# Optimization experiments

Hardware: AMD Instinct MI355X
Metric: run time of the kernel (lower is better)

## Reference

```python
import jax, jax.numpy as jnp
import numpy as np

B, L = 4, 2048
D_MODEL, D_STATE, D_CONV, EXPAND = 1024, 16, 4, 2
D_INNER = D_MODEL * EXPAND


def setup_inputs() -> dict:
    key = jax.random.key(0)
    ks = jax.random.split(key, 6)
    x = jax.random.normal(ks[0], (B, L, D_MODEL), dtype=jnp.float32)
    W_in = jax.random.normal(ks[1], (D_MODEL, 2 * D_INNER), dtype=jnp.float32) / np.sqrt(D_MODEL)
    conv_w = jax.random.normal(ks[2], (D_INNER, D_CONV), dtype=jnp.float32) / np.sqrt(D_CONV)
    conv_b = jax.random.normal(ks[3], (D_INNER,), dtype=jnp.float32) * 0.02
    W_x = jax.random.normal(ks[4], (D_INNER, 2 * D_STATE + 1), dtype=jnp.float32) / np.sqrt(D_INNER)
    A_log = jnp.log(jnp.arange(1, D_STATE + 1, dtype=jnp.float32))
    D_param = jnp.ones((D_INNER,), dtype=jnp.float32)
    W_out = jax.random.normal(ks[5], (D_INNER, D_MODEL), dtype=jnp.float32) / np.sqrt(D_INNER)
    return {"x": x, "W_in": W_in, "conv_w": conv_w, "conv_b": conv_b,
            "W_x": W_x, "A_log": A_log, "D_param": D_param, "W_out": W_out}


def _silu(v):
    return v * jax.nn.sigmoid(v)


def reference(x, W_in, conv_w, conv_b, W_x, A_log, D_param, W_out):
    b, l, _ = x.shape
    # input projection and split into ssm branch and gate
    xz = x @ W_in                                   # (b, l, 2*d_inner)
    x_ssm, z = jnp.split(xz, 2, axis=-1)            # each (b, l, d_inner)
    # depthwise causal conv1d (kernel D_CONV, left pad D_CONV-1, truncate to l)
    xp = jnp.pad(x_ssm, ((0, 0), (D_CONV - 1, 0), (0, 0)))
    xc = conv_b
    for k in range(D_CONV):                         # small fixed kernel loop
        xc = xc + xp[:, k:k + l, :] * conv_w[:, k]
    xc = _silu(xc)                                  # (b, l, d_inner)
    # input-dependent delta, B, C
    x_dbl = xc @ W_x                                # (b, l, 2*d_state+1)
    delta = jax.nn.softplus(x_dbl[..., :1])         # (b, l, 1)
    B_mat = x_dbl[..., 1:1 + D_STATE]               # (b, l, n)
    C_mat = x_dbl[..., 1 + D_STATE:]                # (b, l, n)
    A = -jnp.exp(A_log)                             # (n,)
    A_bar = jnp.exp(delta * A)                      # (b, l, n)
    B_bar = delta * B_mat                           # (b, l, n)

    def step(h, inp):
        a, bb, xt, ct = inp                         # (b,n),(b,n),(b,d),(b,n)
        h = a[:, None, :] * h + bb[:, None, :] * xt[:, :, None]  # (b,d,n)
        y = jnp.einsum('bdn,bn->bd', h, ct)
        return h, y

    h0 = jnp.zeros((b, D_INNER, D_STATE), dtype=x.dtype)
    seq = (jnp.swapaxes(A_bar, 0, 1), jnp.swapaxes(B_bar, 0, 1),
           jnp.swapaxes(xc, 0, 1), jnp.swapaxes(C_mat, 0, 1))
    _, ys = jax.lax.scan(step, h0, seq)             # (l, b, d_inner)
    y = jnp.swapaxes(ys, 0, 1)
    y = y + xc * D_param                            # skip connection
    y = y * _silu(z)                                # gating
    return y @ W_out                                # (b, l, d_model)
```

## Files before the change

### kernel.cpp

```cpp
#include <hip/hip_runtime.h>
#include <hip/hip_bf16.h>
#include <math.h>

typedef __hip_bfloat16 bf16;
typedef __attribute__((ext_vector_type(8))) short short8;
typedef __attribute__((ext_vector_type(4))) float f32x4;

#define BATCH   4
#define L_SEQ   2048
#define DMODEL  1024
#define DSTATE  16
#define DCONV   4
#define DINNER  2048
#define M_ROWS  (BATCH * L_SEQ)

#define CHUNK   64
#define NCH     (L_SEQ / CHUNK)
#define PSTR    52
#define NX      33
#define KSPL    4

__device__ __forceinline__ float b2f(bf16 v) { return __bfloat162float(v); }
__device__ __forceinline__ bf16  f2b(float v) { return __float2bfloat16(v); }
__device__ __forceinline__ float us2f(unsigned short u) {
    return __uint_as_float(((unsigned)u) << 16);
}
__device__ __forceinline__ float ldany(const void* p, int i, int f32) {
    return f32 ? ((const float*)p)[i] : b2f(((const bf16*)p)[i]);
}
__device__ __forceinline__ void load_lds16(const void* g, void* l) {
    __builtin_amdgcn_global_load_lds(
        (const __attribute__((address_space(1))) unsigned int*)g,
        (__attribute__((address_space(3))) unsigned int*)l, 16, 0, 0);
}

union V8 { float4 f4; unsigned short us[8]; };

__global__ void detect_dtype(const unsigned int* __restrict__ alog_bits,
                             int* __restrict__ flag)
{
    *flag = (alog_bits[0] == 0u) ? 1 : 0;
}

__global__ __launch_bounds__(256) void convert_bf16(
    const void* __restrict__ src, bf16* __restrict__ dst, int n,
    const int* __restrict__ flag)
{
    const int f = *flag;
    int i = blockIdx.x * 256 + threadIdx.x;
    if (i < n) dst[i] = f2b(ldany(src, i, f));
}

__global__ __launch_bounds__(256) void transpose_any(
    const void* __restrict__ src, bf16* __restrict__ dst,
    int R, int C, const int* __restrict__ flag)
{
    const int f = *flag;
    __shared__ float tile[32][33];
    int tx = threadIdx.x & 31;
    int ty = threadIdx.x >> 5;
    int c0 = blockIdx.x * 32;
    int r0 = blockIdx.y * 32;
    #pragma unroll
    for (int i = 0; i < 4; i++) {
        int r = r0 + ty + i * 8;
        tile[ty + i * 8][tx] = ldany(src, r * C + c0 + tx, f);
    }
    __syncthreads();
    #pragma unroll
    for (int i = 0; i < 4; i++) {
        int cr = c0 + ty + i * 8;
        dst[(size_t)cr * R + r0 + tx] = f2b(tile[tx][ty + i * 8]);
    }
}

__global__ __launch_bounds__(256) void gemm_mfma(
    const bf16* __restrict__ A, const bf16* __restrict__ Bt,
    void* __restrict__ C1v, void* __restrict__ C2v,
    int M, int N, int Kfull, int split,
    const int* __restrict__ flag, int oMode, int K)
{
    const int fo = (oMode == 2) ? 1 : (oMode & *flag);
    __shared__ __align__(16) bf16 As[128 * 32];
    __shared__ __align__(16) bf16 Bs[128 * 32];
    const int tid  = threadIdx.x;
    const int lane = tid & 63;
    const int w    = tid >> 6;
    const int wr   = w & 1, wc = w >> 1;
    const int m0   = blockIdx.y * 128;
    const int n0   = blockIdx.x * 128;
    const int kz   = blockIdx.z;
    const int kst  = kz * K;

    void* C1 = C1v;
    void* C2 = C2v;
    if (kz) { C1 = (char*)C1v + (size_t)kz * M * N * 4; C2 = C1; }

    f32x4 acc[4][4] = {};

    const int ldr = lane >> 2;
    const int ldc = (lane & 3) * 8;
    const int mrow = lane & 15;
    const int qk   = (lane >> 4) * 8;

    for (int k0 = kst; k0 < kst + K; k0 += 32) {
        __syncthreads();
        #pragma unroll
        for (int j = 0; j < 2; j++) {
            int rg = w * 2 + j;
            int r  = rg * 16 + ldr;
            load_lds16(A  + (size_t)(m0 + r) * Kfull + k0 + ldc, (char*)As + rg * 1024);
            load_lds16(Bt + (size_t)(n0 + r) * Kfull + k0 + ldc, (char*)Bs + rg * 1024);
        }
        __syncthreads();

        short8 af[4], bfr[4];
        #pragma unroll
        for (int i = 0; i < 4; i++) {
            af[i]  = *(const short8*)&As[(wr * 64 + i * 16 + mrow) * 32 + qk];
            bfr[i] = *(const short8*)&Bs[(wc * 64 + i * 16 + mrow) * 32 + qk];
        }
        #pragma unroll
        for (int mi = 0; mi < 4; mi++)
            #pragma unroll
            for (int ni = 0; ni < 4; ni++)
                acc[mi][ni] = __builtin_amdgcn_mfma_f32_16x16x32_bf16(
                    af[mi], bfr[ni], acc[mi][ni], 0, 0, 0);
    }

    const int orow = m0 + wr * 64 + (lane >> 4) * 4;
    const int ocol = wc * 64 + (lane & 15);

    if (n0 + 128 <= split) {
        if (fo) {
            float* Cp = (float*)C1 + (size_t)orow * split + n0 + ocol;
            #pragma unroll
            for (int mi = 0; mi < 4; mi++)
                #pragma unroll
                for (int ni = 0; ni < 4; ni++)
                    #pragma unroll
                    for (int r = 0; r < 4; r++)
                        Cp[(size_t)(mi * 16 + r) * split + ni * 16] = acc[mi][ni][r];
        } else {
            bf16* Cp = (bf16*)C1 + (size_t)orow * split + n0 + ocol;
            #pragma unroll
            for (int mi = 0; mi < 4; mi++)
                #pragma unroll
                for (int ni = 0; ni < 4; ni++)
                    #pragma unroll
                    for (int r = 0; r < 4; r++)
                        Cp[(size_t)(mi * 16 + r) * split + ni * 16] = f2b(acc[mi][ni][r]);
        }
    } else if (n0 >= split) {
        const int Nc = N - split;
        if (fo) {
            float* Cp = (float*)C2 + (size_t)orow * Nc + (n0 - split) + ocol;
            #pragma unroll
            for (int mi = 0; mi < 4; mi++)
                #pragma unroll
                for (int ni = 0; ni < 4; ni++)
                    #pragma unroll
                    for (int r = 0; r < 4; r++)
                        Cp[(size_t)(mi * 16 + r) * Nc + ni * 16] = acc[mi][ni][r];
        } else {
            bf16* Cp = (bf16*)C2 + (size_t)orow * Nc + (n0 - split) + ocol;
            #pragma unroll
            for (int mi = 0; mi < 4; mi++)
                #pragma unroll
                for (int ni = 0; ni < 4; ni++)
                    #pragma unroll
                    for (int r = 0; r < 4; r++)
                        Cp[(size_t)(mi * 16 + r) * Nc + ni * 16] = f2b(acc[mi][ni][r]);
        }
    } else {
        #pragma unroll
        for (int mi = 0; mi < 4; mi++)
            #pragma unroll
            for (int ni = 0; ni < 4; ni++)
                #pragma unroll
                for (int r = 0; r < 4; r++) {
                    int row = orow + mi * 16 + r;
                    int col = n0 + ocol + ni * 16;
                    if (col >= N) continue;
                    float v = acc[mi][ni][r];
                    if (col < split) {
                        if (fo) ((float*)C1)[(size_t)row * split + col] = v;
                        else    ((bf16*)C1)[(size_t)row * split + col]  = f2b(v);
                    } else {
                        int c2 = col - split;
                        if (fo) ((float*)C2)[(size_t)row * (N - split) + c2] = v;
                        else    ((bf16*)C2)[(size_t)row * (N - split) + c2]  = f2b(v);
                    }
                }
    }
}

#define CLC 16

__global__ __launch_bounds__(256) void conv_silu_kernel(
    const bf16* __restrict__ x_ssm, const void* __restrict__ conv_w,
    const void* __restrict__ conv_b, bf16* __restrict__ xc,
    const int* __restrict__ flag)
{
    const int f   = *flag;
    const int tid = threadIdx.x;
    const int d0  = tid * 8;
    const int b   = blockIdx.x / (L_SEQ / CLC);
    const int l0  = (blockIdx.x % (L_SEQ / CLC)) * CLC;

    float wk[DCONV][8], bias[8];
    #pragma unroll
    for (int j = 0; j < 8; j++) {
        bias[j] = ldany(conv_b, d0 + j, f);
        #pragma unroll
        for (int k = 0; k < DCONV; k++)
            wk[k][j] = ldany(conv_w, (d0 + j) * DCONV + k, f);
    }

    const size_t rowstr = DINNER;
    const unsigned short* xin = (const unsigned short*)x_ssm;

    float win[3][8];
    #pragma unroll
    for (int r = 0; r < 3; r++) {
        int l = l0 - 3 + r;
        if (l >= 0) {
            V8 v; v.f4 = *(const float4*)(xin + ((size_t)(b * L_SEQ + l)) * rowstr + d0);
            #pragma unroll
            for (int j = 0; j < 8; j++) win[r][j] = us2f(v.us[j]);
        } else {
            #pragma unroll
            for (int j = 0; j < 8; j++) win[r][j] = 0.f;
        }
    }

    #pragma unroll
    for (int t = 0; t < CLC; t++) {
        int l = l0 + t;
        V8 v; v.f4 = *(const float4*)(xin + ((size_t)(b * L_SEQ + l)) * rowstr + d0);
        float cur[8];
        #pragma unroll
        for (int j = 0; j < 8; j++) cur[j] = us2f(v.us[j]);

        V8 o;
        #pragma unroll
        for (int j = 0; j < 8; j++) {
            float s = bias[j];
            s = fmaf(wk[0][j], win[0][j], s);
            s = fmaf(wk[1][j], win[1][j], s);
            s = fmaf(wk[2][j], win[2][j], s);
            s = fmaf(wk[3][j], cur[j],    s);
            float sv = s / (1.f + __expf(-s));
            o.us[j] = (unsigned short)(__bfloat16_as_ushort(f2b(sv)));
        }
        *(float4*)((unsigned short*)xc + ((size_t)(b * L_SEQ + l)) * rowstr + d0) = o.f4;

        #pragma unroll
        for (int j = 0; j < 8; j++) {
            win[0][j] = win[1][j];
            win[1][j] = win[2][j];
            win[2][j] = cur[j];
        }
    }
}

__global__ void transpose_wx(const void* __restrict__ W_x, bf16* __restrict__ W_xT,
                             const int* __restrict__ flag)
{
    const int f = *flag;
    int idx = blockIdx.x * 256 + threadIdx.x;
    if (idx >= NX * DINNER) return;
    int n = idx / DINNER;
    int k = idx - n * DINNER;
    W_xT[idx] = f2b(ldany(W_x, k * NX + n, f));
}

__global__ __launch_bounds__(256) void pack_P(
    const float* __restrict__ xdbl, const void* __restrict__ A_log,
    float* __restrict__ P, const int* __restrict__ flag)
{
    const int f = *flag;
    int i  = blockIdx.x * 256 + threadIdx.x;
    int bl = i >> 4, n = i & 15;
    float x0 = 0.f, bn = 0.f, cn = 0.f;
    #pragma unroll
    for (int s = 0; s < KSPL; s++) {
        const float* row = xdbl + (size_t)s * M_ROWS * NX + (size_t)bl * NX;
        x0 += row[0];
        bn += row[1 + n];
        cn += row[17 + n];
    }
    float delta = (x0 > 20.f) ? x0 : log1pf(expf(x0));
    float Aneg = -expf(ldany(A_log, n, f));
    float* p = P + (size_t)bl * PSTR;
    p[n]      = expf(delta * Aneg);
    p[16 + n] = delta * bn;
    p[32 + n] = cn;
    if (n == 0) p[48] = delta;
}

__global__ __launch_bounds__(256) void scan_phase1(
    const float* __restrict__ P, const bf16* __restrict__ xc,
    float* __restrict__ hstate)
{
    const int blk = blockIdx.x;
    const int b = blk >> 8;
    const int c = (blk >> 3) & 31;
    const int g = blk & 7;
    const int tid = threadIdx.x;
    const int d = g * 256 + tid;

    __shared__ __align__(16) unsigned short sX[CHUNK][256];

    #pragma unroll
    for (int r = 0; r < 16; r++) {
        int i = r * 256 + tid;
        int t = i >> 6;
        int dd = (i & 63) * 4;
        *(ushort4*)&sX[t][dd] = *(const ushort4*)((const unsigned short*)xc +
            ((size_t)(b * L_SEQ) + c * CHUNK + t) * DINNER + g * 256 + dd);
    }
    __syncthreads();

    const float* __restrict__ p = P + ((size_t)(b * L_SEQ) + c * CHUNK) * PSTR;

    float h[16];
    #pragma unroll
    for (int n = 0; n < 16; n++) h[n] = 0.f;

    #pragma unroll 4
    for (int t = 0; t < CHUNK; t++) {
        const float* pt = p + (size_t)t * PSTR;
        float4 a0 = *(const float4*)(pt + 0);
        float4 a1 = *(const float4*)(pt + 4);
        float4 a2 = *(const float4*)(pt + 8);
        float4 a3 = *(const float4*)(pt + 12);
        float4 b0 = *(const float4*)(pt + 16);
        float4 b1 = *(const float4*)(pt + 20);
        float4 b2 = *(const float4*)(pt + 24);
        float4 b3 = *(const float4*)(pt + 28);
        float xv = us2f(sX[t][tid]);
        float av[16] = {a0.x,a0.y,a0.z,a0.w, a1.x,a1.y,a1.z,a1.w,
                        a2.x,a2.y,a2.z,a2.w, a3.x,a3.y,a3.z,a3.w};
        float bv[16] = {b0.x,b0.y,b0.z,b0.w, b1.x,b1.y,b1.z,b1.w,
                        b2.x,b2.y,b2.z,b2.w, b3.x,b3.y,b3.z,b3.w};
        #pragma unroll
        for (int n = 0; n < 16; n++)
            h[n] = fmaf(av[n], h[n], bv[n] * xv);
    }
    float* out = hstate + (((size_t)b * NCH + c) * DINNER + d) * 16;
    #pragma unroll
    for (int q = 0; q < 4; q++)
        *(float4*)&out[q * 4] = *(const float4*)&h[q * 4];
}

__global__ __launch_bounds__(64) void sum_delta(const float* __restrict__ P,
                                                float* __restrict__ S)
{
    int i = blockIdx.x;
    int t = threadIdx.x;
    float v = P[((size_t)((i >> 5) * L_SEQ) + (i & 31) * CHUNK + t) * PSTR + 48];
    #pragma unroll
    for (int off = 32; off > 0; off >>= 1)
        v += __shfl_xor(v, off);
    if (t == 0) S[i] = v;
}

__global__ __launch_bounds__(256) void scan_phase2(
    float* __restrict__ hstate, const float* __restrict__ S,
    const void* __restrict__ A_log, const int* __restrict__ flag)
{
    const int f = *flag;
    const int b = blockIdx.x >> 7;
    const int dg = blockIdx.x & 127;
    const int tid = threadIdx.x;
    const int d = dg * 16 + (tid >> 4);
    const int n = tid & 15;
    const float Aneg = -expf(ldany(A_log, n, f));

    __shared__ float sS[NCH];
    if (tid < NCH) sS[tid] = S[b * NCH + tid];
    __syncthreads();

    float H = 0.f;
    size_t base = ((size_t)b * NCH * DINNER + d) * 16 + n;
    for (int c = 0; c < NCH; c++) {
        size_t idx = base + (size_t)c * (DINNER * 16);
        float hend = hstate[idx];
        hstate[idx] = H;
        H = fmaf(__expf(Aneg * sS[c]), H, hend);
    }
}

__global__ __launch_bounds__(256) void scan_phase3(
    const float* __restrict__ P, const bf16* __restrict__ xc,
    const bf16* __restrict__ z, const void* __restrict__ Dp,
    const float* __restrict__ hstate, bf16* __restrict__ y,
    const int* __restrict__ flag)
{
    const int f = *flag;
    const int blk = blockIdx.x;
    const int b = blk >> 8;
    const int c = (blk >> 3) & 31;
    const int g = blk & 7;
    const int tid = threadIdx.x;
    const int d = g * 256 + tid;

    __shared__ __align__(16) unsigned short sX[CHUNK][256];

    #pragma unroll
    for (int r = 0; r < 16; r++) {
        int i = r * 256 + tid;
        int t = i >> 6;
        int dd = (i & 63) * 4;
        *(ushort4*)&sX[t][dd] = *(const ushort4*)((const unsigned short*)xc +
            ((size_t)(b * L_SEQ) + c * CHUNK + t) * DINNER + g * 256 + dd);
    }
    __syncthreads();

    const float Dd = ldany(Dp, d, f);
    float h[16];
    const float* hin = hstate + (((size_t)b * NCH + c) * DINNER + d) * 16;
    #pragma unroll
    for (int q = 0; q < 4; q++)
        *(float4*)&h[q * 4] = *(const float4*)&hin[q * 4];

    const float* __restrict__ p = P + ((size_t)(b * L_SEQ) + c * CHUNK) * PSTR;
    const size_t ybase = ((size_t)(b * L_SEQ) + c * CHUNK) * DINNER + d;
    const unsigned short* zp = (const unsigned short*)z;

    #pragma unroll 4
    for (int t = 0; t < CHUNK; t++) {
        const float* pt = p + (size_t)t * PSTR;
        float4 a0 = *(const float4*)(pt + 0);
        float4 a1 = *(const float4*)(pt + 4);
        float4 a2 = *(const float4*)(pt + 8);
        float4 a3 = *(const float4*)(pt + 12);
        float4 b0 = *(const float4*)(pt + 16);
        float4 b1 = *(const float4*)(pt + 20);
        float4 b2 = *(const float4*)(pt + 24);
        float4 b3 = *(const float4*)(pt + 28);
        float4 c0 = *(const float4*)(pt + 32);
        float4 c1 = *(const float4*)(pt + 36);
        float4 c2 = *(const float4*)(pt + 40);
        float4 c3 = *(const float4*)(pt + 44);
        float xv = us2f(sX[t][tid]);
        float av[16] = {a0.x,a0.y,a0.z,a0.w, a1.x,a1.y,a1.z,a1.w,
                        a2.x,a2.y,a2.z,a2.w, a3.x,a3.y,a3.z,a3.w};
        float bv[16] = {b0.x,b0.y,b0.z,b0.w, b1.x,b1.y,b1.z,b1.w,
                        b2.x,b2.y,b2.z,b2.w, b3.x,b3.y,b3.z,b3.w};
        float cv[16] = {c0.x,c0.y,c0.z,c0.w, c1.x,c1.y,c1.z,c1.w,
                        c2.x,c2.y,c2.z,c2.w, c3.x,c3.y,c3.z,c3.w};
        float p0 = 0.f, p1 = 0.f;
        #pragma unroll
        for (int n = 0; n < 16; n += 2) {
            h[n]     = fmaf(av[n],     h[n],     bv[n]     * xv);
            h[n + 1] = fmaf(av[n + 1], h[n + 1], bv[n + 1] * xv);
            p0 = fmaf(h[n],     cv[n],     p0);
            p1 = fmaf(h[n + 1], cv[n + 1], p1);
        }
        float zv = us2f(zp[ybase + (size_t)t * DINNER]);
        float yv = (p0 + p1) + xv * Dd;
        float sz = zv / (1.f + __expf(-zv));
        y[ybase + (size_t)t * DINNER] = f2b(yv * sz);
    }
}

extern "C" void kernel_launch(void* const* d_in, const int* in_sizes, int n_in,
                              void* d_out, int out_size, void* d_ws, size_t ws_size,
                              hipStream_t stream)
{
    const void* x      = d_in[0];
    const void* W_in   = d_in[1];
    const void* conv_w = d_in[2];
    const void* conv_b = d_in[3];
    const void* W_x    = d_in[4];
    const void* A_log  = d_in[5];
    const void* Dp     = d_in[6];
    const void* W_out  = d_in[7];

    char* w = (char*)d_ws;
    bf16* x_ssm = (bf16*)w; w += (size_t)M_ROWS * DINNER * 2;
    bf16* z     = (bf16*)w; w += (size_t)M_ROWS * DINNER * 2;
    bf16* xc    = (bf16*)w; w += (size_t)M_ROWS * DINNER * 2;
    bf16* yb    = (bf16*)w; w += (size_t)M_ROWS * DINNER * 2;
    float* P    = (float*)w; w += (size_t)M_ROWS * PSTR * 4;
    int*  flag  = (int*)w;  w += 256;
    float* S    = (float*)w; w += 4096;

    bf16* x_bf    = yb;
    bf16* W_inT   = xc;
    bf16* W_outT  = x_ssm;
    float* hstate = (float*)((char*)x_ssm + (size_t)DMODEL * DINNER * 2);
    float* xdbl  = (float*)yb;
    bf16*  W_xT  = (bf16*)((char*)yb + 8 * 1024 * 1024);

    detect_dtype<<<1, 1, 0, stream>>>((const unsigned int*)A_log, flag);

    convert_bf16<<<(M_ROWS * DMODEL) / 256, 256, 0, stream>>>(x, x_bf, M_ROWS * DMODEL, flag);
    transpose_any<<<dim3((2 * DINNER) / 32, DMODEL / 32), 256, 0, stream>>>(
        W_in, W_inT, DMODEL, 2 * DINNER, flag);

    gemm_mfma<<<dim3((2 * DINNER) / 128, M_ROWS / 128), 256, 0, stream>>>(
        x_bf, W_inT, x_ssm, z, M_ROWS, 2 * DINNER, DMODEL, DINNER, flag, 0, DMODEL);

    conv_silu_kernel<<<BATCH * (L_SEQ / CLC), 256, 0, stream>>>(
        x_ssm, conv_w, conv_b, xc, flag);

    transpose_any<<<dim3(DMODEL / 32, DINNER / 32), 256, 0, stream>>>(
        W_out, W_outT, DINNER, DMODEL, flag);

    transpose_wx<<<(NX * DINNER + 255) / 256, 256, 0, stream>>>(W_x, W_xT, flag);
    gemm_mfma<<<dim3(1, M_ROWS / 128, KSPL), 256, 0, stream>>>(
        xc, W_xT, xdbl, xdbl, M_ROWS, NX, DINNER, NX, flag, 2, DINNER / KSPL);
    pack_P<<<(M_ROWS * 16) / 256, 256, 0, stream>>>(xdbl, A_log, P, flag);

    scan_phase1<<<BATCH * NCH * 8, 256, 0, stream>>>(P, xc, hstate);
    sum_delta<<<BATCH * NCH, 64, 0, stream>>>(P, S);
    scan_phase2<<<BATCH * 128, 256, 0, stream>>>(hstate, S, A_log, flag);
    scan_phase3<<<BATCH * NCH * 8, 256, 0, stream>>>(P, xc, z, Dp, hstate, yb, flag);

    gemm_mfma<<<dim3(DMODEL / 128, M_ROWS / 128), 256, 0, stream>>>(
        yb, W_outT, d_out, d_out, M_ROWS, DMODEL, DINNER, DMODEL, flag, 1, DINNER);
}
```

Before: 408.7 us.

## Double-buffer GEMM LDS tiles and XOR-swizzle LDS layout

The MFMA GEMM now keeps two LDS buffers for A and B tiles and issues the next k-tile's global-to-LDS loads before computing on the current tile. This overlaps memory latency with MFMA work and drops one barrier per iteration. It also XOR-swizzles the column offset within each 16-row group to reduce LDS bank conflicts on the fragment reads. In exchange, LDS use per block doubles, which may lower occupancy. Correctness also depends on the direct-to-LDS loads finishing before the single barrier at the end of each iteration.

```diff
diff --git a/kernel.cpp b/kernel.cpp
--- a/kernel.cpp
+++ b/kernel.cpp
@@ -81,8 +81,8 @@
     const int* __restrict__ flag, int oMode, int K)
 {
     const int fo = (oMode == 2) ? 1 : (oMode & *flag);
-    __shared__ __align__(16) bf16 As[128 * 32];
-    __shared__ __align__(16) bf16 Bs[128 * 32];
+    __shared__ __align__(16) bf16 As[2][128 * 32];
+    __shared__ __align__(16) bf16 Bs[2][128 * 32];
     const int tid  = threadIdx.x;
     const int lane = tid & 63;
     const int w    = tid >> 6;
@@ -98,27 +98,49 @@
 
     f32x4 acc[4][4] = {};
 
-    const int ldr = lane >> 2;
-    const int ldc = (lane & 3) * 8;
+    const int ldr  = lane >> 2;
+    const int ldc  = ((lane & 3) ^ ((lane >> 2) & 3) ^ ((lane >> 4) & 3)) * 8;
     const int mrow = lane & 15;
-    const int qk   = (lane >> 4) * 8;
-
-    for (int k0 = kst; k0 < kst + K; k0 += 32) {
-        __syncthreads();
-        #pragma unroll
-        for (int j = 0; j < 2; j++) {
-            int rg = w * 2 + j;
-            int r  = rg * 16 + ldr;
-            load_lds16(A  + (size_t)(m0 + r) * Kfull + k0 + ldc, (char*)As + rg * 1024);
-            load_lds16(Bt + (size_t)(n0 + r) * Kfull + k0 + ldc, (char*)Bs + rg * 1024);
-        }
-        __syncthreads();
-
+    const int qksw = ((lane >> 4) ^ (lane & 3) ^ ((lane >> 2) & 3)) * 8;
+
+    const bf16* aptr[2];
+    const bf16* bptr[2];
+    #pragma unroll
+    for (int j = 0; j < 2; j++) {
+        int r = (w * 2 + j) * 16 + ldr;
+        aptr[j] = A  + (size_t)(m0 + r) * Kfull + kst + ldc;
+        bptr[j] = Bt + (size_t)(n0 + r) * Kfull + kst + ldc;
+    }
+
+    const int iters = K / 32;
+    #pragma unroll
+    for (int j = 0; j < 2; j++) {
+        int rg = w * 2 + j;
+        load_lds16(aptr[j], (char*)As[0] + rg * 1024);
+        load_lds16(bptr[j], (char*)Bs[0] + rg * 1024);
+        aptr[j] += 32;
+        bptr[j] += 32;
+    }
+    __syncthreads();
+
+    for (int it = 0; it < iters; it++) {
+        const int cur = it & 1;
+        if (it + 1 < iters) {
+            const int nxt = cur ^ 1;
+            #pragma unroll
+            for (int j = 0; j < 2; j++) {
+                int rg = w * 2 + j;
+                load_lds16(aptr[j], (char*)As[nxt] + rg * 1024);
+                load_lds16(bptr[j], (char*)Bs[nxt] + rg * 1024);
+                aptr[j] += 32;
+                bptr[j] += 32;
+            }
+        }
         short8 af[4], bfr[4];
         #pragma unroll
         for (int i = 0; i < 4; i++) {
-            af[i]  = *(const short8*)&As[(wr * 64 + i * 16 + mrow) * 32 + qk];
-            bfr[i] = *(const short8*)&Bs[(wc * 64 + i * 16 + mrow) * 32 + qk];
+            af[i]  = *(const short8*)&As[cur][(wr * 64 + i * 16 + mrow) * 32 + qksw];
+            bfr[i] = *(const short8*)&Bs[cur][(wc * 64 + i * 16 + mrow) * 32 + qksw];
         }
         #pragma unroll
         for (int mi = 0; mi < 4; mi++)
@@ -126,6 +148,7 @@
             for (int ni = 0; ni < 4; ni++)
                 acc[mi][ni] = __builtin_amdgcn_mfma_f32_16x16x32_bf16(
                     af[mi], bfr[ni], acc[mi][ni], 0, 0, 0);
+        __syncthreads();
     }
 
     const int orow = m0 + wr * 64 + (lane >> 4) * 4;
```

Measured after the change: 387.9 us. 5.1% less time.
